# Kernel tuning notes

Hardware: AMD Instinct MI355X
Metric: run time of the kernel (lower is better)

The kernel has to match this reference:

```python
import jax, jax.numpy as jnp
import numpy as np

EPS = 1e-06

def setup_inputs() -> dict:
    key = jax.random.key(0)
    kx, kq, kk, kv = jax.random.split(key, 4)
    B, S, D, F = 8, 4096, 1024, 1024
    # glorot-uniform-ish scale for weights
    scale = (6.0 / (D + F)) ** 0.5
    x = jax.random.normal(kx, (B, S, D), dtype=jnp.float32)
    Wq = jax.random.uniform(kq, (D, F), dtype=jnp.float32, minval=-scale, maxval=scale)
    Wk = jax.random.uniform(kk, (D, F), dtype=jnp.float32, minval=-scale, maxval=scale)
    Wv = jax.random.uniform(kv, (D, F), dtype=jnp.float32, minval=-scale, maxval=scale)
    return {"x": x, "Wq": Wq, "Wk": Wk, "Wv": Wv}


def reference(x, Wq, Wk, Wv):
    # x: [B, S, D]; projections -> [B, S, F]
    queries = jnp.einsum('bsd,df->bsf', x, Wq)
    keys = jnp.einsum('bsd,df->bsf', x, Wk)
    values = jnp.einsum('bsd,df->bsf', x, Wv)
    # feature map: relu(.) + 1 (strictly positive kernel features)
    queries = jax.nn.relu(queries) + 1.0
    keys = jax.nn.relu(keys) + 1.0
    # numerator: K^T V over sequence -> [B, F, F]
    numerator = jnp.einsum('bsf,bsg->bfg', keys, values)
    # denominator: sum of keys over sequence -> [B, 1, F]; broadcasts over last axis
    denominator = jnp.sum(keys, axis=-2, keepdims=True)
    context = numerator / (denominator + EPS)
    # output: context @ Q^T -> [B, F, S]
    output = jnp.einsum('bfg,bsg->bfs', context, queries)
    return output
```

## Files before the change

kernel.cpp:

```cpp
#include <hip/hip_runtime.h>


#define EPSF 1e-6f

constexpr int Bb = 8;
constexpr int Ss = 4096;
constexpr int Dd = 1024;
constexpr int Ff = 1024;

typedef __attribute__((ext_vector_type(8))) short   bf16x8;
typedef __attribute__((ext_vector_type(8))) unsigned short u16x8;
typedef __attribute__((ext_vector_type(4))) float   f32x4;

typedef __attribute__((address_space(3))) unsigned char lds_u8;
typedef __attribute__((address_space(3))) const bf16x8  lds_cvec;

static __device__ __forceinline__ unsigned short f2bf(float f) {
    union { float f; unsigned int u; } v; v.f = f;
    unsigned int r = (v.u + 0x7fffu + ((v.u >> 16) & 1u)) >> 16;
    return (unsigned short)r;
}
static __device__ __forceinline__ float bf2f(unsigned short u) {
    union { unsigned int u; float f; } v; v.u = ((unsigned int)u) << 16;
    return v.f;
}

static __device__ __forceinline__ void gld_lds16(const void* g, lds_u8* l) {
    __builtin_amdgcn_global_load_lds(
        (const __attribute__((address_space(1))) unsigned int*)g,
        (__attribute__((address_space(3))) unsigned int*)l,
        16, 0, 0);
}

__global__ void cvt_x_kernel(const float* __restrict__ x, unsigned short* __restrict__ xb, int n4)
{
    int i = blockIdx.x * blockDim.x + threadIdx.x;
    if (i >= n4) return;
    float4 v = *(const float4*)&x[(size_t)i * 4];
    ushort4 o;
    o.x = f2bf(v.x); o.y = f2bf(v.y); o.z = f2bf(v.z); o.w = f2bf(v.w);
    *(ushort4*)&xb[(size_t)i * 4] = o;
}

__global__ void cvt_wT_kernel(const float* __restrict__ Wq,
                              const float* __restrict__ Wk,
                              const float* __restrict__ Wv,
                              unsigned short* __restrict__ WT)
{
    const int z = blockIdx.z;
    const float* __restrict__ W = (z == 0) ? Wq : (z == 1 ? Wk : Wv);
    unsigned short* __restrict__ dst = WT + (size_t)z * Dd * Ff;

    __shared__ float tile[32][33];
    const int tid = threadIdx.x;
    const int d0 = blockIdx.y * 32, f0 = blockIdx.x * 32;
    const int c = tid & 31, r8 = tid >> 5;
#pragma unroll
    for (int p = 0; p < 4; ++p) {
        int r = p * 8 + r8;
        tile[r][c] = W[(size_t)(d0 + r) * Ff + f0 + c];
    }
    __syncthreads();
#pragma unroll
    for (int p = 0; p < 4; ++p) {
        int r = p * 8 + r8;
        dst[(size_t)(f0 + r) * Dd + d0 + c] = f2bf(tile[c][r]);
    }
}

__global__ void add_ctx_kernel(const unsigned short* __restrict__ p,
                               unsigned short* __restrict__ c,
                               const float* __restrict__ den)
{
    const int b = blockIdx.y;
    const size_t i8 = ((size_t)blockIdx.x * 256 + threadIdx.x) * 8;
    const int g0 = (int)(i8 & (size_t)(Ff - 1));
    const u16x8 a0 = *(const u16x8*)(p + (size_t)(2 * b) * Ff * Ff + i8);
    const u16x8 a1 = *(const u16x8*)(p + (size_t)(2 * b + 1) * Ff * Ff + i8);
    const float4 d0 = *(const float4*)&den[(size_t)b * Ff + g0];
    const float4 d1 = *(const float4*)&den[(size_t)b * Ff + g0 + 4];
    const float dv[8] = {d0.x, d0.y, d0.z, d0.w, d1.x, d1.y, d1.z, d1.w};
    u16x8 o;
#pragma unroll
    for (int j = 0; j < 8; ++j)
        o[j] = f2bf((bf2f(a0[j]) + bf2f(a1[j])) * (1.f / (dv[j] + EPSF)));
    *(u16x8*)(c + (size_t)b * Ff * Ff + i8) = o;
}

template<int ACT, int SCALE, int OUT_BF16, int SPLITK2, int DENACC, int QKV>
__global__ __launch_bounds__(512, 2)
void gemm8(const unsigned short* __restrict__ A,
           const unsigned short* __restrict__ Bt,
           void* __restrict__ Cout,
           const float* __restrict__ den,
           float* __restrict__ denw,
           int lda, int ldb, int ldc, int Kdim,
           size_t strideA, size_t strideB, size_t strideC)
{
    __shared__ __align__(16) unsigned char smem_[131072];
    lds_u8* const smem = (lds_u8*)smem_;

    const int gx = gridDim.x, gxy = gx * gridDim.y;
    int flat = blockIdx.z * gxy + blockIdx.y * gx + blockIdx.x;
    const int nwg = gxy * gridDim.z;
    const int cpx = nwg >> 3;
    flat = (flat & 7) * cpx + (flat >> 3);
    const int z = flat / gxy;
    const int rem = flat - z * gxy;
    const int by = rem / gx;
    const int bx = rem - by * gx;

    const int pid  = QKV ? (z % 3) : 0;
    const int zb   = QKV ? (z / 3) : (SPLITK2 ? (z >> 1) : z);
    const int koff = SPLITK2 ? ((z & 1) * Kdim) : 0;

    const unsigned short* __restrict__ Ag;
    const unsigned short* __restrict__ Bg;
    int bm, bn, ldcr;
    size_t coff;
    bool actv, dacc;
    if (QKV) {
        if (pid == 0) {
            Ag = Bt + (size_t)zb * Ss * Dd;
            Bg = A;
            bm = bx * 256; bn = by * 256;
            ldcr = Ff;
            coff = (size_t)zb * Ss * Ff;
            actv = true;  dacc = false;
        } else {
            Ag = A + (size_t)pid * Dd * Ff;
            Bg = Bt + (size_t)zb * Ss * Dd;
            bm = by * 256; bn = bx * 256;
            ldcr = Ss;
            coff = ((size_t)pid * Bb + zb) * ((size_t)Ff * Ss);
            actv = (pid == 1); dacc = (pid == 1);
        }
    } else {
        Ag = A + strideA * zb + koff;
        Bg = Bt + strideB * zb + koff;
        bm = by * 256; bn = bx * 256;
        ldcr = ldc;
        coff = strideC * (size_t)z;
        actv = ACT; dacc = DENACC;
    }
    const float* __restrict__ denb = SCALE ? (den + (size_t)zb * Ff) : nullptr;

    const int tid  = threadIdx.x;
    const int wv   = tid >> 6, lane = tid & 63;
    const int wm   = wv >> 2, wn = wv & 3;
    const int lm   = lane & 15;
    const int kg16 = (lane >> 4) << 4;
    const int swz  = (lm & 7) << 4;
    const int kbs  = (((tid & 7) ^ ((tid >> 3) & 7)) << 4);
    const int srow = tid >> 3;

    f32x4 acc[8][4];
#pragma unroll
    for (int i = 0; i < 8; ++i)
#pragma unroll
        for (int j = 0; j < 4; ++j) acc[i][j] = (f32x4){0.f, 0.f, 0.f, 0.f};

    lds_u8* const A0 = smem;
    lds_u8* const B0 = smem + 32768;
    lds_u8* const A1 = smem + 65536;
    lds_u8* const B1 = smem + 98304;

    auto STAGE = [&](int ts, int m, int buf, int h) {
        const unsigned short* gb = m ? Bg : Ag;
        const int ld = m ? ldb : lda;
        const int off0 = m ? bn : bm;
        lds_u8* lb = smem + buf * 65536 + m * 32768 + h * 16384 + wv * 1024;
#pragma unroll
        for (int q = 0; q < 2; ++q) {
            int row = h * 128 + q * 64 + srow;
            const unsigned char* g =
                (const unsigned char*)(gb + (size_t)(off0 + row) * ld + ts * 64) + kbs;
            gld_lds16(g, lb + q * 8192);
        }
    };
    auto LDA4 = [&](bf16x8* dst, int fmb, int kk, lds_u8* Ab) {
#pragma unroll
        for (int f = 0; f < 4; ++f) {
            int r = wm * 128 + (fmb + f) * 16 + lm;
            dst[f] = *(lds_cvec*)(Ab + r * 128 + ((kk * 64 + kg16) ^ swz));
        }
    };
    auto LDB4 = [&](bf16x8* dst, int kk, lds_u8* Bb) {
#pragma unroll
        for (int f = 0; f < 4; ++f) {
            int c = wn * 64 + f * 16 + lm;
            dst[f] = *(lds_cvec*)(Bb + c * 128 + ((kk * 64 + kg16) ^ swz));
        }
    };

#define MM16(a4, b4, mo)                                                        \
    do {                                                                        \
        __builtin_amdgcn_s_setprio(1);                                          \
        _Pragma("unroll")                                                       \
        for (int fm = 0; fm < 4; ++fm)                                          \
            _Pragma("unroll")                                                   \
            for (int fn = 0; fn < 4; ++fn)                                      \
                acc[(mo) + fm][fn] = __builtin_amdgcn_mfma_f32_16x16x32_bf16(   \
                    (b4)[fn], (a4)[fm], acc[(mo) + fm][fn], 0, 0, 0);           \
        __builtin_amdgcn_s_setprio(0);                                          \
    } while (0)

#define PHEND()                                                     \
    do {                                                            \
        asm volatile("s_waitcnt lgkmcnt(0)");                       \
        __builtin_amdgcn_sched_barrier(0);                          \
        __builtin_amdgcn_s_barrier();                               \
    } while (0)
#define PHEND_VM2()                                                 \
    do {                                                            \
        asm volatile("s_waitcnt vmcnt(2) lgkmcnt(0)");              \
        __builtin_amdgcn_sched_barrier(0);                          \
        __builtin_amdgcn_s_barrier();                               \
    } while (0)

    const int NT = Kdim >> 6;
    const int NI = NT >> 1;

    STAGE(0, 1, 0, 0); STAGE(0, 1, 0, 1);
    STAGE(0, 0, 0, 0); STAGE(0, 0, 0, 1);
    STAGE(1, 1, 1, 0); STAGE(1, 1, 1, 1);
    asm volatile("s_waitcnt vmcnt(4)");
    __builtin_amdgcn_s_barrier();

    bf16x8 a03[4], a47[4], b0[4], b1[4];
    LDB4(b0, 0, B0); LDA4(a03, 0, 0, A0);

    for (int i = 0; i < NI; ++i) {
        const int t = 2 * i;
        const int t1s = t + 1;
        const int t2s = (t + 2 < NT) ? t + 2 : NT - 1;
        const int t3s = (t + 3 < NT) ? t + 3 : NT - 1;

        STAGE(t1s, 0, 1, 0);
        LDA4(a47, 4, 0, A0);
        MM16(a03, b0, 0);
        PHEND();
        STAGE(t1s, 0, 1, 1);
        LDA4(a03, 0, 1, A0); LDB4(b1, 1, B0);
        MM16(a47, b0, 4);
        PHEND();
        STAGE(t2s, 1, 0, 0);
        LDA4(a47, 4, 1, A0);
        MM16(a03, b1, 0);
        PHEND_VM2();
        STAGE(t2s, 1, 0, 1);
        LDA4(a03, 0, 0, A1); LDB4(b0, 0, B1);
        MM16(a47, b1, 4);
        PHEND();
        STAGE(t2s, 0, 0, 0);
        LDA4(a47, 4, 0, A1);
        MM16(a03, b0, 0);
        PHEND();
        STAGE(t2s, 0, 0, 1);
        LDA4(a03, 0, 1, A1); LDB4(b1, 1, B1);
        MM16(a47, b0, 4);
        PHEND();
        STAGE(t3s, 1, 1, 0);
        LDA4(a47, 4, 1, A1);
        MM16(a03, b1, 0);
        PHEND_VM2();
        STAGE(t3s, 1, 1, 1);
        LDA4(a03, 0, 0, A0); LDB4(b0, 0, B0);
        MM16(a47, b1, 4);
        PHEND();
    }

    asm volatile("s_waitcnt vmcnt(0)");

    const int hi4 = (lane >> 4) * 4;
#pragma unroll
    for (int fm = 0; fm < 8; ++fm) {
        const int gr = bm + wm * 128 + fm * 16 + lm;
        float rowsum = 0.f;
#pragma unroll
        for (int fn = 0; fn < 4; ++fn) {
            const int gcn = bn + wn * 64 + fn * 16 + hi4;
            f32x4 v = acc[fm][fn];
            if (actv) {
#pragma unroll
                for (int e = 0; e < 4; ++e) v[e] = fmaxf(v[e], 0.f) + 1.f;
            }
            if (dacc) rowsum += v[0] + v[1] + v[2] + v[3];
            if (SCALE) {
                float4 d4 = *(const float4*)&denb[gcn];
                v[0] *= 1.f / (d4.x + EPSF);
                v[1] *= 1.f / (d4.y + EPSF);
                v[2] *= 1.f / (d4.z + EPSF);
                v[3] *= 1.f / (d4.w + EPSF);
            }
            if (OUT_BF16) {
                ushort4 o;
                o.x = f2bf(v[0]); o.y = f2bf(v[1]); o.z = f2bf(v[2]); o.w = f2bf(v[3]);
                *(ushort4*)((unsigned short*)Cout + coff + (size_t)gr * ldcr + gcn) = o;
            } else {
                *(float4*)((float*)Cout + coff + (size_t)gr * ldcr + gcn) =
                    *(float4*)&v;
            }
        }
        if (dacc) {
            rowsum += __shfl_xor(rowsum, 16, 64);
            rowsum += __shfl_xor(rowsum, 32, 64);
            if (lane < 16) atomicAdd(denw + (size_t)zb * Ff + gr, rowsum);
        }
    }
#undef MM16
#undef PHEND
#undef PHEND_VM2
}

extern "C" void kernel_launch(void* const* d_in, const int* in_sizes, int n_in,
                              void* d_out, int out_size, void* d_ws, size_t ws_size,
                              hipStream_t stream)
{
    (void)in_sizes; (void)n_in; (void)out_size;
    const float* x  = (const float*)d_in[0];
    const float* Wq = (const float*)d_in[1];
    const float* Wk = (const float*)d_in[2];
    const float* Wv = (const float*)d_in[3];
    float* out = (float*)d_out;

    const size_t nx   = (size_t)Bb * Ss * Dd;
    const size_t nW   = (size_t)3 * Dd * Ff;
    const size_t nQKV = (size_t)Bb * Ss * Ff;
    const size_t nCtx = (size_t)Bb * Ff * Ff;
    const size_t nP   = (size_t)16 * Ff * Ff;

    unsigned short* xb   = (unsigned short*)d_ws;
    unsigned short* WT   = xb + nx;
    unsigned short* Qb   = WT + nW;
    unsigned short* KbT  = Qb + nQKV;
    unsigned short* VbT  = KbT + nQKV;
    unsigned short* ctxb = VbT + nQKV;
    float* den = (float*)(ctxb + nCtx);
    unsigned short* pctx = (unsigned short*)(den + (size_t)Bb * Ff);

    const size_t need_split =
        ((nx + nW + 3 * nQKV + nCtx + nP) * 2 + (size_t)Bb * Ff * 4);
    const bool do_split = ws_size >= need_split;

    hipMemsetAsync(den, 0, (size_t)Bb * Ff * sizeof(float), stream);

    cvt_x_kernel<<<dim3((int)(nx / 4 / 256)), 256, 0, stream>>>(x, xb, (int)(nx / 4));
    cvt_wT_kernel<<<dim3(Ff / 32, Dd / 32, 3), 256, 0, stream>>>(Wq, Wk, Wv, WT);

    gemm8<0, 0, 1, 0, 0, 1><<<dim3(Ss / 256, Ff / 256, 3 * Bb), 512, 0, stream>>>(
        WT, xb, Qb, nullptr, den,
        Dd, Dd, 0, Dd, 0, 0, 0);

    if (do_split) {
        gemm8<0, 0, 1, 1, 0, 0><<<dim3(Ff / 256, Ff / 256, 2 * Bb), 512, 0, stream>>>(
            KbT, VbT, pctx, nullptr, nullptr,
            Ss, Ss, Ff, Ss / 2, (size_t)Ff * Ss, (size_t)Ff * Ss, (size_t)Ff * Ff);
        add_ctx_kernel<<<dim3(Ff * Ff / 8 / 256, Bb), 256, 0, stream>>>(pctx, ctxb, den);
    } else {
        gemm8<0, 1, 1, 0, 0, 0><<<dim3(Ff / 256, Ff / 256, Bb), 512, 0, stream>>>(
            KbT, VbT, ctxb, den, nullptr,
            Ss, Ss, Ff, Ss, (size_t)Ff * Ss, (size_t)Ff * Ss, (size_t)Ff * Ff);
    }

    gemm8<0, 0, 0, 0, 0, 0><<<dim3(Ss / 256, Ff / 256, Bb), 512, 0, stream>>>(
        ctxb, Qb, out, nullptr, nullptr,
        Ff, Ff, Ss, Ff, (size_t)Ff * Ff, (size_t)Ss * Ff, (size_t)Ff * Ss);
}
```

Before: 406.6 us.

## Fuse prep kernels and remap GEMM tile order for L2 locality

Merges the x conversion, weight transpose and den zeroing into one prep kernel, which removes two launches and a memset. It also changes the block-to-tile mapping in the QKV GEMM so that the three projections of the same tile are adjacent after XCD swizzling. The output GEMM gets a new mode that groups 4x4 tile supertiles per batch so operands are shared better in cache. This aims at launch overhead and L2 reuse, and brings more index arithmetic and a hardcoded grid size in exchange.

```diff
diff --git a/kernel.cpp b/kernel.cpp
--- a/kernel.cpp
+++ b/kernel.cpp
@@ -32,39 +32,45 @@
         16, 0, 0);
 }
 
-__global__ void cvt_x_kernel(const float* __restrict__ x, unsigned short* __restrict__ xb, int n4)
+__global__ __launch_bounds__(256)
+void prep_kernel(const float* __restrict__ x,
+                 const float* __restrict__ Wq,
+                 const float* __restrict__ Wk,
+                 const float* __restrict__ Wv,
+                 unsigned short* __restrict__ xb,
+                 unsigned short* __restrict__ WT,
+                 float* __restrict__ den)
 {
-    int i = blockIdx.x * blockDim.x + threadIdx.x;
-    if (i >= n4) return;
-    float4 v = *(const float4*)&x[(size_t)i * 4];
-    ushort4 o;
-    o.x = f2bf(v.x); o.y = f2bf(v.y); o.z = f2bf(v.z); o.w = f2bf(v.w);
-    *(ushort4*)&xb[(size_t)i * 4] = o;
-}
-
-__global__ void cvt_wT_kernel(const float* __restrict__ Wq,
-                              const float* __restrict__ Wk,
-                              const float* __restrict__ Wv,
-                              unsigned short* __restrict__ WT)
-{
-    const int z = blockIdx.z;
-    const float* __restrict__ W = (z == 0) ? Wq : (z == 1 ? Wk : Wv);
-    unsigned short* __restrict__ dst = WT + (size_t)z * Dd * Ff;
-
     __shared__ float tile[32][33];
+    const int bid = blockIdx.x;
     const int tid = threadIdx.x;
-    const int d0 = blockIdx.y * 32, f0 = blockIdx.x * 32;
-    const int c = tid & 31, r8 = tid >> 5;
-#pragma unroll
-    for (int p = 0; p < 4; ++p) {
-        int r = p * 8 + r8;
-        tile[r][c] = W[(size_t)(d0 + r) * Ff + f0 + c];
-    }
-    __syncthreads();
-#pragma unroll
-    for (int p = 0; p < 4; ++p) {
-        int r = p * 8 + r8;
-        dst[(size_t)(f0 + r) * Dd + d0 + c] = f2bf(tile[c][r]);
+    if (bid < 32768) {
+        const int i = bid * 256 + tid;
+        float4 v = *(const float4*)&x[(size_t)i * 4];
+        ushort4 o;
+        o.x = f2bf(v.x); o.y = f2bf(v.y); o.z = f2bf(v.z); o.w = f2bf(v.w);
+        *(ushort4*)&xb[(size_t)i * 4] = o;
+    } else if (bid < 35840) {
+        const int w = bid - 32768;
+        const int z = w >> 10;
+        const int r = w & 1023;
+        const int d0 = (r >> 5) * 32, f0 = (r & 31) * 32;
+        const float* __restrict__ W = (z == 0) ? Wq : (z == 1 ? Wk : Wv);
+        unsigned short* __restrict__ dst = WT + (size_t)z * Dd * Ff;
+        const int c = tid & 31, r8 = tid >> 5;
+#pragma unroll
+        for (int p = 0; p < 4; ++p) {
+            int rr = p * 8 + r8;
+            tile[rr][c] = W[(size_t)(d0 + rr) * Ff + f0 + c];
+        }
+        __syncthreads();
+#pragma unroll
+        for (int p = 0; p < 4; ++p) {
+            int rr = p * 8 + r8;
+            dst[(size_t)(f0 + rr) * Dd + d0 + c] = f2bf(tile[c][rr]);
+        }
+    } else {
+        for (int i = tid; i < Bb * Ff; i += 256) den[i] = 0.f;
     }
 }
 
@@ -87,7 +93,7 @@
     *(u16x8*)(c + (size_t)b * Ff * Ff + i8) = o;
 }
 
-template<int ACT, int SCALE, int OUT_BF16, int SPLITK2, int DENACC, int QKV>
+template<int ACT, int SCALE, int OUT_BF16, int SPLITK2, int DENACC, int MODE>
 __global__ __launch_bounds__(512, 2)
 void gemm8(const unsigned short* __restrict__ A,
            const unsigned short* __restrict__ Bt,
@@ -105,37 +111,51 @@
     const int nwg = gxy * gridDim.z;
     const int cpx = nwg >> 3;
     flat = (flat & 7) * cpx + (flat >> 3);
-    const int z = flat / gxy;
-    const int rem = flat - z * gxy;
-    const int by = rem / gx;
-    const int bx = rem - by * gx;
-
-    const int pid  = QKV ? (z % 3) : 0;
-    const int zb   = QKV ? (z / 3) : (SPLITK2 ? (z >> 1) : z);
-    const int koff = SPLITK2 ? ((z & 1) * Kdim) : 0;
-
+
+    int pid = 0, zb = 0, bm, bn, ldcr;
+    size_t coff, koff = 0;
+    bool actv, dacc;
     const unsigned short* __restrict__ Ag;
     const unsigned short* __restrict__ Bg;
-    int bm, bn, ldcr;
-    size_t coff;
-    bool actv, dacc;
-    if (QKV) {
+
+    if (MODE == 1) {
+        pid = flat % 3;
+        int q = flat / 3;
+        const int byq = q & 3;  q >>= 2;
+        const int bxq = q & 15; zb = q >> 4;
         if (pid == 0) {
             Ag = Bt + (size_t)zb * Ss * Dd;
             Bg = A;
-            bm = bx * 256; bn = by * 256;
+            bm = bxq * 256; bn = byq * 256;
             ldcr = Ff;
             coff = (size_t)zb * Ss * Ff;
             actv = true;  dacc = false;
         } else {
             Ag = A + (size_t)pid * Dd * Ff;
             Bg = Bt + (size_t)zb * Ss * Dd;
-            bm = by * 256; bn = bx * 256;
+            bm = byq * 256; bn = bxq * 256;
             ldcr = Ss;
             coff = ((size_t)pid * Bb + zb) * ((size_t)Ff * Ss);
             actv = (pid == 1); dacc = (pid == 1);
         }
+    } else if (MODE == 2) {
+        zb = flat >> 6;
+        const int r = flat & 63;
+        const int sg = r >> 4, i = r & 15;
+        const int bxq = sg * 4 + (i & 3), byq = i >> 2;
+        Ag = A + strideA * zb;
+        Bg = Bt + strideB * zb;
+        bm = byq * 256; bn = bxq * 256;
+        ldcr = ldc;
+        coff = strideC * (size_t)zb;
+        actv = false; dacc = false;
     } else {
+        const int z = flat / gxy;
+        const int rem = flat - z * gxy;
+        const int by = rem / gx;
+        const int bx = rem - by * gx;
+        zb   = SPLITK2 ? (z >> 1) : z;
+        koff = SPLITK2 ? (size_t)((z & 1) * Kdim) : 0;
         Ag = A + strideA * zb + koff;
         Bg = Bt + strideB * zb + koff;
         bm = by * 256; bn = bx * 256;
@@ -343,10 +363,7 @@
         ((nx + nW + 3 * nQKV + nCtx + nP) * 2 + (size_t)Bb * Ff * 4);
     const bool do_split = ws_size >= need_split;
 
-    hipMemsetAsync(den, 0, (size_t)Bb * Ff * sizeof(float), stream);
-
-    cvt_x_kernel<<<dim3((int)(nx / 4 / 256)), 256, 0, stream>>>(x, xb, (int)(nx / 4));
-    cvt_wT_kernel<<<dim3(Ff / 32, Dd / 32, 3), 256, 0, stream>>>(Wq, Wk, Wv, WT);
+    prep_kernel<<<dim3(35841), 256, 0, stream>>>(x, Wq, Wk, Wv, xb, WT, den);
 
     gemm8<0, 0, 1, 0, 0, 1><<<dim3(Ss / 256, Ff / 256, 3 * Bb), 512, 0, stream>>>(
         WT, xb, Qb, nullptr, den,
@@ -363,7 +380,7 @@
             Ss, Ss, Ff, Ss, (size_t)Ff * Ss, (size_t)Ff * Ss, (size_t)Ff * Ff);
     }
 
-    gemm8<0, 0, 0, 0, 0, 0><<<dim3(Ss / 256, Ff / 256, Bb), 512, 0, stream>>>(
+    gemm8<0, 0, 0, 0, 0, 2><<<dim3(Ss / 256, Ff / 256, Bb), 512, 0, stream>>>(
         ctxb, Qb, out, nullptr, nullptr,
         Ff, Ff, Ss, Ff, (size_t)Ff * Ff, (size_t)Ss * Ff, (size_t)Ff * Ss);
 }
```

Result: no change. 407.1 us (+0.1%).
